# Kernel optimization log

Hardware: AMD Instinct MI355X
Metric: run time of the kernel (lower is better)

Reference implementation:

```python
import jax, jax.numpy as jnp
import numpy as np

E, K, D = 50000, 8, 256
NH = 4
HD = D // NH
SCALE = HD ** -0.5
EPS = 1e-8


def setup_inputs() -> dict:
    key = jax.random.key(0)
    ks = jax.random.split(key, 16)
    p = lambda k, shp: (jax.random.normal(k, shp, dtype=jnp.float32) * 0.02)
    return {
        "x_i": jax.random.normal(ks[0], (E, D), dtype=jnp.float32),
        "x_j": jax.random.normal(ks[1], (E, D), dtype=jnp.float32),
        "h_seq_i": jax.random.normal(ks[2], (E, K, D), dtype=jnp.float32),
        "h_seq_j": jax.random.normal(ks[3], (E, K, D), dtype=jnp.float32),
        "edge_emb": jax.random.normal(ks[4], (E, D), dtype=jnp.float32),
        "Wq": p(ks[5], (D, D)), "bq": jnp.zeros((D,), jnp.float32),
        "Wk": p(ks[6], (D, D)), "bk": jnp.zeros((D,), jnp.float32),
        "We1": p(ks[7], (D, D // 2)), "be1": jnp.zeros((D // 2,), jnp.float32),
        "We2": p(ks[8], (D // 2, 1)), "be2": jnp.zeros((1,), jnp.float32),
        "Wo1": p(ks[9], (3, 16)), "bo1": jnp.zeros((16,), jnp.float32),
        "Wo2": p(ks[10], (16, 1)), "bo2": jnp.zeros((1,), jnp.float32),
    }


def reference(x_i, x_j, h_seq_i, h_seq_j, edge_emb,
              Wq, bq, Wk, bk, We1, be1, We2, be2, Wo1, bo1, Wo2, bo2):
    # (A) attribute alignment: cosine similarity mapped to (0,1)
    num = jnp.sum(x_i * x_j, axis=-1)
    den = jnp.maximum(jnp.linalg.norm(x_i, axis=-1), EPS) * \
          jnp.maximum(jnp.linalg.norm(x_j, axis=-1), EPS)
    attr_score = (num / den + 1.0) / 2.0  # [E]

    # (B) activity alignment: tiny cross-attention, mean of softmax diagonal
    Q = (jnp.einsum('ekd,df->ekf', h_seq_i, Wq) + bq).reshape(E, K, NH, HD)
    Kv = (jnp.einsum('ekd,df->ekf', h_seq_j, Wk) + bk).reshape(E, K, NH, HD)
    scores = jnp.einsum('eqhd,ekhd->ehqk', Q, Kv) * SCALE  # [E,NH,K,K]
    attn = jax.nn.softmax(scores, axis=-1)
    diag = jnp.diagonal(attn, axis1=-2, axis2=-1)  # [E,NH,K]
    activity_score = diag.mean(axis=(-1, -2))  # [E]

    # (C) edge plausibility MLP (exact GELU as in torch default)
    h = jax.nn.gelu(edge_emb @ We1 + be1, approximate=False)
    edge_score = jax.nn.sigmoid((h @ We2 + be2)[..., 0])  # [E]

    signals = jnp.stack([attr_score, activity_score, edge_score], axis=-1)  # [E,3]
    out = jax.nn.gelu(signals @ Wo1 + bo1, approximate=False) @ Wo2 + bo2
    return jax.nn.sigmoid(out[..., 0])  # [E]
```

## Files before the change

### kernel.cpp

```cpp
#include <hip/hip_runtime.h>

#define E_TOT   50000
#define DD      256
#define TE      4
#define NGROUP  (E_TOT / TE)
#define SCALE_V 0.125f

typedef __attribute__((ext_vector_type(4))) float f32x4;
typedef __attribute__((ext_vector_type(8))) short short8;

__device__ __forceinline__ unsigned short f2bf(float f) {
    unsigned u = __float_as_uint(f);
    u += 0x7fffu + ((u >> 16) & 1u);
    return (unsigned short)(u >> 16);
}
__device__ __forceinline__ float gelu_exact(float x) {
    return 0.5f * x * (1.0f + erff(x * 0.70710678118654752440f));
}
__device__ __forceinline__ float sigmoidf(float x) {
    return 1.0f / (1.0f + __expf(-x));
}

__device__ __forceinline__ f32x4 aload(const float* p) {
    f32x4 r;
    asm volatile("global_load_dwordx4 %0, %1, off" : "=v"(r) : "v"(p));
    return r;
}
#define WAITV(N) do { asm volatile("s_waitcnt vmcnt(" #N ")" ::: "memory"); \
                      __builtin_amdgcn_sched_barrier(0); } while (0)

__global__ void prep_weights(const float* __restrict__ Wq,
                             const float* __restrict__ Wk,
                             const float* __restrict__ We1,
                             unsigned short* __restrict__ wqT,
                             unsigned short* __restrict__ wkT,
                             unsigned short* __restrict__ w1T) {
    int i = blockIdx.x * 256 + threadIdx.x;
    if (i < 65536) {
        int k = i >> 8, n = i & 255;
        wqT[n * 256 + k] = f2bf(Wq[i]);
    } else if (i < 131072) {
        int j = i - 65536;
        int k = j >> 8, n = j & 255;
        wkT[n * 256 + k] = f2bf(Wk[j]);
    } else {
        int j = i - 131072;
        int k = j >> 7, n = j & 127;
        w1T[n * 256 + k] = f2bf(We1[j]);
    }
}

__device__ __forceinline__ void proj_gemm(const unsigned short (*A)[260],
                                          const unsigned short* __restrict__ Wt,
                                          f32x4 acc[2][4], int lr, int lq, int w) {
    #pragma unroll
    for (int ks = 0; ks < 8; ++ks) {
        short8 a0 = *(const short8*)&A[lr][ks * 32 + lq * 8];
        short8 a1 = *(const short8*)&A[16 + lr][ks * 32 + lq * 8];
        #pragma unroll
        for (int n = 0; n < 4; ++n) {
            const int col = (w * 4 + n) * 16 + lr;
            short8 bv = *(const short8*)(Wt + col * 256 + ks * 32 + lq * 8);
            acc[0][n] = __builtin_amdgcn_mfma_f32_16x16x32_bf16(a0, bv, acc[0][n], 0, 0, 0);
            acc[1][n] = __builtin_amdgcn_mfma_f32_16x16x32_bf16(a1, bv, acc[1][n], 0, 0, 0);
        }
    }
}

__device__ __forceinline__ void writeback(unsigned short (*T)[260],
                                          const f32x4 acc[2][4],
                                          const float* __restrict__ bias,
                                          int lr, int lq, int w) {
    #pragma unroll
    for (int n = 0; n < 4; ++n) {
        const int col = (w * 4 + n) * 16 + lr;
        const float bs = bias[col];
        #pragma unroll
        for (int m = 0; m < 2; ++m) {
            #pragma unroll
            for (int v = 0; v < 4; ++v) {
                const int row = m * 16 + lq * 4 + v;
                T[row][col] = f2bf(acc[m][n][v] + bs);
            }
        }
    }
}

__global__ __launch_bounds__(256, 3)
void fused_all(const float* __restrict__ x_i,
               const float* __restrict__ x_j,
               const float* __restrict__ h_i,
               const float* __restrict__ h_j,
               const float* __restrict__ emb,
               const unsigned short* __restrict__ wqT,
               const unsigned short* __restrict__ wkT,
               const unsigned short* __restrict__ w1T,
               const float* __restrict__ bq,
               const float* __restrict__ bk,
               const float* __restrict__ be1,
               const float* __restrict__ We2,
               const float* __restrict__ be2,
               const float* __restrict__ Wo1,
               const float* __restrict__ bo1,
               const float* __restrict__ Wo2,
               const float* __restrict__ bo2,
               float* __restrict__ out) {
    __shared__ unsigned short tI[32][260];
    __shared__ unsigned short tJ[32][260];
    __shared__ float sEmb[TE][DD];
    __shared__ float sEdgeP[4][4];

    const int t  = threadIdx.x;
    const int w  = t >> 6;
    const int l  = t & 63;
    const int lr = l & 15, lq = l >> 4;
    const int g  = blockIdx.x;
    const int e  = g * TE + w;
    const size_t hbase = (size_t)g * (TE * 8 * DD);

    f32x4 si[8], sj[8];
    #pragma unroll
    for (int i = 0; i < 8; ++i)
        si[i] = aload(h_i + hbase + (size_t)(i * 256 + t) * 4);
    #pragma unroll
    for (int i = 0; i < 8; ++i)
        sj[i] = aload(h_j + hbase + (size_t)(i * 256 + t) * 4);
    f32x4 xa = aload(x_i + (size_t)e * DD + l * 4);
    f32x4 xb = aload(x_j + (size_t)e * DD + l * 4);
    f32x4 em = aload(emb + ((size_t)g * TE + (t >> 6)) * DD + (t & 63) * 4);
    __builtin_amdgcn_sched_barrier(0);

    WAITV(11);
    #pragma unroll
    for (int i = 0; i < 8; ++i) {
        const int f = i * 256 + t;
        *(ushort4*)&tI[f >> 6][(f & 63) * 4] =
            make_ushort4(f2bf(si[i][0]), f2bf(si[i][1]), f2bf(si[i][2]), f2bf(si[i][3]));
    }
    WAITV(3);
    #pragma unroll
    for (int i = 0; i < 8; ++i) {
        const int f = i * 256 + t;
        *(ushort4*)&tJ[f >> 6][(f & 63) * 4] =
            make_ushort4(f2bf(sj[i][0]), f2bf(sj[i][1]), f2bf(sj[i][2]), f2bf(sj[i][3]));
    }
    WAITV(0);
    *(f32x4*)&sEmb[t >> 6][(t & 63) * 4] = em;
    float cd = xa[0]*xb[0] + xa[1]*xb[1] + xa[2]*xb[2] + xa[3]*xb[3];
    float ci = xa[0]*xa[0] + xa[1]*xa[1] + xa[2]*xa[2] + xa[3]*xa[3];
    float cj = xb[0]*xb[0] + xb[1]*xb[1] + xb[2]*xb[2] + xb[3]*xb[3];
    __syncthreads();

    f32x4 accE[2] = {};
    {
        #pragma unroll
        for (int ks = 0; ks < 8; ++ks) {
            f32x4 e0 = *(const f32x4*)&sEmb[lr & 3][ks * 32 + lq * 8];
            f32x4 e1 = *(const f32x4*)&sEmb[lr & 3][ks * 32 + lq * 8 + 4];
            short8 ae;
            ae[0] = (short)f2bf(e0[0]); ae[1] = (short)f2bf(e0[1]);
            ae[2] = (short)f2bf(e0[2]); ae[3] = (short)f2bf(e0[3]);
            ae[4] = (short)f2bf(e1[0]); ae[5] = (short)f2bf(e1[1]);
            ae[6] = (short)f2bf(e1[2]); ae[7] = (short)f2bf(e1[3]);
            #pragma unroll
            for (int n = 0; n < 2; ++n) {
                const int col = w * 32 + n * 16 + lr;
                short8 bv = *(const short8*)(w1T + col * 256 + ks * 32 + lq * 8);
                accE[n] = __builtin_amdgcn_mfma_f32_16x16x32_bf16(ae, bv, accE[n], 0, 0, 0);
            }
        }
    }
    {
        f32x4 accQ[2][4] = {};
        proj_gemm(tI, wqT, accQ, lr, lq, w);
        __syncthreads();
        writeback(tI, accQ, bq, lr, lq, w);
    }
    {
        f32x4 accK[2][4] = {};
        proj_gemm(tJ, wkT, accK, lr, lq, w);
        __syncthreads();
        writeback(tJ, accK, bk, lr, lq, w);
    }
    {
        float p[4] = {0.f, 0.f, 0.f, 0.f};
        #pragma unroll
        for (int n = 0; n < 2; ++n) {
            const int col = w * 32 + n * 16 + lr;
            const float b1 = be1[col], w2 = We2[col];
            #pragma unroll
            for (int v = 0; v < 4; ++v)
                p[v] += gelu_exact(accE[n][v] + b1) * w2;
        }
        #pragma unroll
        for (int off = 1; off < 16; off <<= 1) {
            #pragma unroll
            for (int v = 0; v < 4; ++v) p[v] += __shfl_xor(p[v], off);
        }
        if (l == 0) {
            sEdgeP[w][0] = p[0]; sEdgeP[w][1] = p[1];
            sEdgeP[w][2] = p[2]; sEdgeP[w][3] = p[3];
        }
    }
    __syncthreads();

    float contrib = 0.f;
    #pragma unroll
    for (int h = 0; h < 4; ++h) {
        f32x4 s = {};
        #pragma unroll
        for (int ks = 0; ks < 2; ++ks) {
            short8 a = *(const short8*)&tJ[w * 8 + (lr & 7)][h * 64 + ks * 32 + lq * 8];
            short8 b = *(const short8*)&tI[w * 8 + (lr & 7)][h * 64 + ks * 32 + lq * 8];
            s = __builtin_amdgcn_mfma_f32_16x16x32_bf16(a, b, s, 0, 0, 0);
        }
        float sc[4];
        #pragma unroll
        for (int v = 0; v < 4; ++v) sc[v] = s[v] * SCALE_V;
        float m4 = fmaxf(fmaxf(sc[0], sc[1]), fmaxf(sc[2], sc[3]));
        float mx = fmaxf(m4, __shfl_xor(m4, 16));
        float pe[4], ps = 0.f;
        #pragma unroll
        for (int v = 0; v < 4; ++v) { pe[v] = __expf(sc[v] - mx); ps += pe[v]; }
        float tot = ps + __shfl_xor(ps, 16);
        float pd = 0.f;
        #pragma unroll
        for (int v = 0; v < 4; ++v)
            pd = (((lq * 4 + v) & 7) == (lr & 7)) ? pe[v] : pd;
        if (lr < 8 && lq < 2) contrib += pd / tot;
    }

    #pragma unroll
    for (int off = 1; off < 64; off <<= 1) {
        contrib += __shfl_xor(contrib, off);
        cd += __shfl_xor(cd, off);
        ci += __shfl_xor(ci, off);
        cj += __shfl_xor(cj, off);
    }
    const float act  = contrib * (1.0f / 32.0f);
    const float attr = (cd / (fmaxf(sqrtf(ci), 1e-8f) * fmaxf(sqrtf(cj), 1e-8f))
                        + 1.0f) * 0.5f;
    const float es = sigmoidf(sEdgeP[0][w] + sEdgeP[1][w] + sEdgeP[2][w] +
                              sEdgeP[3][w] + be2[0]);

    float r = 0.f;
    if (l < 16) {
        float z = attr * Wo1[l] + act * Wo1[16 + l] + es * Wo1[32 + l] + bo1[l];
        r = gelu_exact(z) * Wo2[l];
    }
    r += __shfl_xor(r, 1);
    r += __shfl_xor(r, 2);
    r += __shfl_xor(r, 4);
    r += __shfl_xor(r, 8);
    if (l == 0) out[e] = sigmoidf(r + bo2[0]);
}

extern "C" void kernel_launch(void* const* d_in, const int* in_sizes, int n_in,
                              void* d_out, int out_size, void* d_ws, size_t ws_size,
                              hipStream_t stream) {
    const float* x_i  = (const float*)d_in[0];
    const float* x_j  = (const float*)d_in[1];
    const float* h_i  = (const float*)d_in[2];
    const float* h_j  = (const float*)d_in[3];
    const float* emb  = (const float*)d_in[4];
    const float* Wq   = (const float*)d_in[5];
    const float* bq   = (const float*)d_in[6];
    const float* Wk   = (const float*)d_in[7];
    const float* bk   = (const float*)d_in[8];
    const float* We1  = (const float*)d_in[9];
    const float* be1  = (const float*)d_in[10];
    const float* We2  = (const float*)d_in[11];
    const float* be2  = (const float*)d_in[12];
    const float* Wo1  = (const float*)d_in[13];
    const float* bo1  = (const float*)d_in[14];
    const float* Wo2  = (const float*)d_in[15];
    const float* bo2  = (const float*)d_in[16];
    float* out = (float*)d_out;

    unsigned short* wqT = (unsigned short*)d_ws;
    unsigned short* wkT = wqT + 65536;
    unsigned short* w1T = wkT + 65536;

    prep_weights<<<640, 256, 0, stream>>>(Wq, Wk, We1, wqT, wkT, w1T);
    fused_all<<<NGROUP, 256, 0, stream>>>(x_i, x_j, h_i, h_j, emb,
                                          wqT, wkT, w1T,
                                          bq, bk, be1, We2, be2,
                                          Wo1, bo1, Wo2, bo2, out);
}
```

Measured before the change: 607.5 us.

## Pre-convert activations to bf16 MFMA fragment layout in a separate pass

Adds a conversion kernel that rewrites h_seq_i, h_seq_j and edge_emb into bf16 arrays laid out as MFMA A-fragments in workspace. A new fused kernel then loads these fragments directly from global memory, skipping the LDS staging and conversion, and raises occupancy to 4. The old kernel stays as a fallback when the workspace is too small, with padded sEmb rows. The extra pass adds a full read of the fp32 inputs plus a write and re-read of the bf16 copies.

```diff
diff --git a/kernel.cpp b/kernel.cpp
--- a/kernel.cpp
+++ b/kernel.cpp
@@ -6,6 +6,9 @@
 #define NGROUP  (E_TOT / TE)
 #define SCALE_V 0.125f
 
+#define NHCHUNK 12800000
+#define NECHUNK 1600000
+
 typedef __attribute__((ext_vector_type(4))) float f32x4;
 typedef __attribute__((ext_vector_type(8))) short short8;
 
@@ -20,14 +23,6 @@
 __device__ __forceinline__ float sigmoidf(float x) {
     return 1.0f / (1.0f + __expf(-x));
 }
-
-__device__ __forceinline__ f32x4 aload(const float* p) {
-    f32x4 r;
-    asm volatile("global_load_dwordx4 %0, %1, off" : "=v"(r) : "v"(p));
-    return r;
-}
-#define WAITV(N) do { asm volatile("s_waitcnt vmcnt(" #N ")" ::: "memory"); \
-                      __builtin_amdgcn_sched_barrier(0); } while (0)
 
 __global__ void prep_weights(const float* __restrict__ Wq,
                              const float* __restrict__ Wk,
@@ -50,6 +45,229 @@
     }
 }
 
+__global__ void conv_frag(const float* __restrict__ hi,
+                          const float* __restrict__ hj,
+                          const float* __restrict__ emb,
+                          unsigned short* __restrict__ fi,
+                          unsigned short* __restrict__ fj,
+                          unsigned short* __restrict__ ebf) {
+    const int nthr = gridDim.x * blockDim.x;
+    const int tid  = blockIdx.x * blockDim.x + threadIdx.x;
+
+    for (int c = tid; c < NHCHUNK; c += nthr) {
+        const int g  = c >> 10;
+        const int r  = c & 1023;
+        const int ks = r >> 7, m = (r >> 6) & 1, l = r & 63;
+        const size_t row = (size_t)g * 32 + m * 16 + (l & 15);
+        const int    col = ks * 32 + (l >> 4) * 8;
+        const float* pi = hi + row * DD + col;
+        const float* pj = hj + row * DD + col;
+        f32x4 a0 = *(const f32x4*)pi;
+        f32x4 a1 = *(const f32x4*)(pi + 4);
+        f32x4 b0 = *(const f32x4*)pj;
+        f32x4 b1 = *(const f32x4*)(pj + 4);
+        ushort4 ua0 = make_ushort4(f2bf(a0[0]), f2bf(a0[1]), f2bf(a0[2]), f2bf(a0[3]));
+        ushort4 ua1 = make_ushort4(f2bf(a1[0]), f2bf(a1[1]), f2bf(a1[2]), f2bf(a1[3]));
+        ushort4 ub0 = make_ushort4(f2bf(b0[0]), f2bf(b0[1]), f2bf(b0[2]), f2bf(b0[3]));
+        ushort4 ub1 = make_ushort4(f2bf(b1[0]), f2bf(b1[1]), f2bf(b1[2]), f2bf(b1[3]));
+        *(ushort4*)(fi + (size_t)c * 8)     = ua0;
+        *(ushort4*)(fi + (size_t)c * 8 + 4) = ua1;
+        *(ushort4*)(fj + (size_t)c * 8)     = ub0;
+        *(ushort4*)(fj + (size_t)c * 8 + 4) = ub1;
+    }
+    for (int c = tid; c < NECHUNK; c += nthr) {
+        const float* p = emb + (size_t)c * 8;
+        f32x4 a0 = *(const f32x4*)p;
+        f32x4 a1 = *(const f32x4*)(p + 4);
+        *(ushort4*)(ebf + (size_t)c * 8)     =
+            make_ushort4(f2bf(a0[0]), f2bf(a0[1]), f2bf(a0[2]), f2bf(a0[3]));
+        *(ushort4*)(ebf + (size_t)c * 8 + 4) =
+            make_ushort4(f2bf(a1[0]), f2bf(a1[1]), f2bf(a1[2]), f2bf(a1[3]));
+    }
+}
+
+__device__ __forceinline__ void writeback(unsigned short (*T)[260],
+                                          const f32x4 acc[2][4],
+                                          const float* __restrict__ bias,
+                                          int lr, int lq, int w) {
+    #pragma unroll
+    for (int n = 0; n < 4; ++n) {
+        const int col = (w * 4 + n) * 16 + lr;
+        const float bs = bias[col];
+        #pragma unroll
+        for (int m = 0; m < 2; ++m) {
+            #pragma unroll
+            for (int v = 0; v < 4; ++v) {
+                const int row = m * 16 + lq * 4 + v;
+                T[row][col] = f2bf(acc[m][n][v] + bs);
+            }
+        }
+    }
+}
+
+__global__ __launch_bounds__(256, 4)
+void fused_direct(const float* __restrict__ x_i,
+                  const float* __restrict__ x_j,
+                  const unsigned short* __restrict__ fi,
+                  const unsigned short* __restrict__ fj,
+                  const unsigned short* __restrict__ ebf,
+                  const unsigned short* __restrict__ wqT,
+                  const unsigned short* __restrict__ wkT,
+                  const unsigned short* __restrict__ w1T,
+                  const float* __restrict__ bq,
+                  const float* __restrict__ bk,
+                  const float* __restrict__ be1,
+                  const float* __restrict__ We2,
+                  const float* __restrict__ be2,
+                  const float* __restrict__ Wo1,
+                  const float* __restrict__ bo1,
+                  const float* __restrict__ Wo2,
+                  const float* __restrict__ bo2,
+                  float* __restrict__ out) {
+    __shared__ unsigned short tI[32][260];
+    __shared__ unsigned short tJ[32][260];
+    __shared__ float sEdgeP[4][4];
+
+    const int t  = threadIdx.x;
+    const int w  = t >> 6;
+    const int l  = t & 63;
+    const int lr = l & 15, lq = l >> 4;
+    const int g  = blockIdx.x;
+    const int e  = g * TE + w;
+
+    f32x4 xa = *(const f32x4*)(x_i + (size_t)e * DD + l * 4);
+    f32x4 xb = *(const f32x4*)(x_j + (size_t)e * DD + l * 4);
+    float cd = xa[0]*xb[0] + xa[1]*xb[1] + xa[2]*xb[2] + xa[3]*xb[3];
+    float ci = xa[0]*xa[0] + xa[1]*xa[1] + xa[2]*xa[2] + xa[3]*xa[3];
+    float cj = xb[0]*xb[0] + xb[1]*xb[1] + xb[2]*xb[2] + xb[3]*xb[3];
+
+    {
+        const unsigned short* fb = fi + (size_t)g * 8192;
+        f32x4 acc[2][4] = {};
+        #pragma unroll
+        for (int ks = 0; ks < 8; ++ks) {
+            short8 a0 = *(const short8*)(fb + ks * 1024 + l * 8);
+            short8 a1 = *(const short8*)(fb + ks * 1024 + 512 + l * 8);
+            #pragma unroll
+            for (int n = 0; n < 4; ++n) {
+                const int col = (w * 4 + n) * 16 + lr;
+                short8 bv = *(const short8*)(wqT + col * 256 + ks * 32 + lq * 8);
+                acc[0][n] = __builtin_amdgcn_mfma_f32_16x16x32_bf16(a0, bv, acc[0][n], 0, 0, 0);
+                acc[1][n] = __builtin_amdgcn_mfma_f32_16x16x32_bf16(a1, bv, acc[1][n], 0, 0, 0);
+            }
+        }
+        writeback(tI, acc, bq, lr, lq, w);
+    }
+    {
+        const unsigned short* fb = fj + (size_t)g * 8192;
+        f32x4 acc[2][4] = {};
+        #pragma unroll
+        for (int ks = 0; ks < 8; ++ks) {
+            short8 a0 = *(const short8*)(fb + ks * 1024 + l * 8);
+            short8 a1 = *(const short8*)(fb + ks * 1024 + 512 + l * 8);
+            #pragma unroll
+            for (int n = 0; n < 4; ++n) {
+                const int col = (w * 4 + n) * 16 + lr;
+                short8 bv = *(const short8*)(wkT + col * 256 + ks * 32 + lq * 8);
+                acc[0][n] = __builtin_amdgcn_mfma_f32_16x16x32_bf16(a0, bv, acc[0][n], 0, 0, 0);
+                acc[1][n] = __builtin_amdgcn_mfma_f32_16x16x32_bf16(a1, bv, acc[1][n], 0, 0, 0);
+            }
+        }
+        writeback(tJ, acc, bk, lr, lq, w);
+    }
+    {
+        f32x4 accE[2] = {};
+        const unsigned short* er = ebf + (size_t)g * 1024 + (lr & 3) * 256;
+        #pragma unroll
+        for (int ks = 0; ks < 8; ++ks) {
+            short8 ae = *(const short8*)(er + ks * 32 + lq * 8);
+            #pragma unroll
+            for (int n = 0; n < 2; ++n) {
+                const int col = w * 32 + n * 16 + lr;
+                short8 bv = *(const short8*)(w1T + col * 256 + ks * 32 + lq * 8);
+                accE[n] = __builtin_amdgcn_mfma_f32_16x16x32_bf16(ae, bv, accE[n], 0, 0, 0);
+            }
+        }
+        float p[4] = {0.f, 0.f, 0.f, 0.f};
+        #pragma unroll
+        for (int n = 0; n < 2; ++n) {
+            const int col = w * 32 + n * 16 + lr;
+            const float b1 = be1[col], w2 = We2[col];
+            #pragma unroll
+            for (int v = 0; v < 4; ++v)
+                p[v] += gelu_exact(accE[n][v] + b1) * w2;
+        }
+        #pragma unroll
+        for (int off = 1; off < 16; off <<= 1) {
+            #pragma unroll
+            for (int v = 0; v < 4; ++v) p[v] += __shfl_xor(p[v], off);
+        }
+        if (l == 0) {
+            sEdgeP[w][0] = p[0]; sEdgeP[w][1] = p[1];
+            sEdgeP[w][2] = p[2]; sEdgeP[w][3] = p[3];
+        }
+    }
+    __syncthreads();
+
+    float contrib = 0.f;
+    #pragma unroll
+    for (int h = 0; h < 4; ++h) {
+        f32x4 s = {};
+        #pragma unroll
+        for (int ks = 0; ks < 2; ++ks) {
+            short8 a = *(const short8*)&tJ[w * 8 + (lr & 7)][h * 64 + ks * 32 + lq * 8];
+            short8 b = *(const short8*)&tI[w * 8 + (lr & 7)][h * 64 + ks * 32 + lq * 8];
+            s = __builtin_amdgcn_mfma_f32_16x16x32_bf16(a, b, s, 0, 0, 0);
+        }
+        float sc[4];
+        #pragma unroll
+        for (int v = 0; v < 4; ++v) sc[v] = s[v] * SCALE_V;
+        float m4 = fmaxf(fmaxf(sc[0], sc[1]), fmaxf(sc[2], sc[3]));
+        float mx = fmaxf(m4, __shfl_xor(m4, 16));
+        float pe[4], ps = 0.f;
+        #pragma unroll
+        for (int v = 0; v < 4; ++v) { pe[v] = __expf(sc[v] - mx); ps += pe[v]; }
+        float tot = ps + __shfl_xor(ps, 16);
+        float pd = 0.f;
+        #pragma unroll
+        for (int v = 0; v < 4; ++v)
+            pd = (((lq * 4 + v) & 7) == (lr & 7)) ? pe[v] : pd;
+        if (lr < 8 && lq < 2) contrib += pd / tot;
+    }
+
+    #pragma unroll
+    for (int off = 1; off < 64; off <<= 1) {
+        contrib += __shfl_xor(contrib, off);
+        cd += __shfl_xor(cd, off);
+        ci += __shfl_xor(ci, off);
+        cj += __shfl_xor(cj, off);
+    }
+    const float act  = contrib * (1.0f / 32.0f);
+    const float attr = (cd / (fmaxf(sqrtf(ci), 1e-8f) * fmaxf(sqrtf(cj), 1e-8f))
+                        + 1.0f) * 0.5f;
+    const float es = sigmoidf(sEdgeP[0][w] + sEdgeP[1][w] + sEdgeP[2][w] +
+                              sEdgeP[3][w] + be2[0]);
+
+    float r = 0.f;
+    if (l < 16) {
+        float z = attr * Wo1[l] + act * Wo1[16 + l] + es * Wo1[32 + l] + bo1[l];
+        r = gelu_exact(z) * Wo2[l];
+    }
+    r += __shfl_xor(r, 1);
+    r += __shfl_xor(r, 2);
+    r += __shfl_xor(r, 4);
+    r += __shfl_xor(r, 8);
+    if (l == 0) out[e] = sigmoidf(r + bo2[0]);
+}
+
+__device__ __forceinline__ f32x4 aload(const float* p) {
+    f32x4 r;
+    asm volatile("global_load_dwordx4 %0, %1, off" : "=v"(r) : "v"(p));
+    return r;
+}
+#define WAITV(N) do { asm volatile("s_waitcnt vmcnt(" #N ")" ::: "memory"); \
+                      __builtin_amdgcn_sched_barrier(0); } while (0)
+
 __device__ __forceinline__ void proj_gemm(const unsigned short (*A)[260],
                                           const unsigned short* __restrict__ Wt,
                                           f32x4 acc[2][4], int lr, int lq, int w) {
@@ -67,47 +285,28 @@
     }
 }
 
-__device__ __forceinline__ void writeback(unsigned short (*T)[260],
-                                          const f32x4 acc[2][4],
-                                          const float* __restrict__ bias,
-                                          int lr, int lq, int w) {
-    #pragma unroll
-    for (int n = 0; n < 4; ++n) {
-        const int col = (w * 4 + n) * 16 + lr;
-        const float bs = bias[col];
-        #pragma unroll
-        for (int m = 0; m < 2; ++m) {
-            #pragma unroll
-            for (int v = 0; v < 4; ++v) {
-                const int row = m * 16 + lq * 4 + v;
-                T[row][col] = f2bf(acc[m][n][v] + bs);
-            }
-        }
-    }
-}
-
 __global__ __launch_bounds__(256, 3)
-void fused_all(const float* __restrict__ x_i,
-               const float* __restrict__ x_j,
-               const float* __restrict__ h_i,
-               const float* __restrict__ h_j,
-               const float* __restrict__ emb,
-               const unsigned short* __restrict__ wqT,
-               const unsigned short* __restrict__ wkT,
-               const unsigned short* __restrict__ w1T,
-               const float* __restrict__ bq,
-               const float* __restrict__ bk,
-               const float* __restrict__ be1,
-               const float* __restrict__ We2,
-               const float* __restrict__ be2,
-               const float* __restrict__ Wo1,
-               const float* __restrict__ bo1,
-               const float* __restrict__ Wo2,
-               const float* __restrict__ bo2,
-               float* __restrict__ out) {
+void fused_legacy(const float* __restrict__ x_i,
+                  const float* __restrict__ x_j,
+                  const float* __restrict__ h_i,
+                  const float* __restrict__ h_j,
+                  const float* __restrict__ emb,
+                  const unsigned short* __restrict__ wqT,
+                  const unsigned short* __restrict__ wkT,
+                  const unsigned short* __restrict__ w1T,
+                  const float* __restrict__ bq,
+                  const float* __restrict__ bk,
+                  const float* __restrict__ be1,
+                  const float* __restrict__ We2,
+                  const float* __restrict__ be2,
+                  const float* __restrict__ Wo1,
+                  const float* __restrict__ bo1,
+                  const float* __restrict__ Wo2,
+                  const float* __restrict__ bo2,
+                  float* __restrict__ out) {
     __shared__ unsigned short tI[32][260];
     __shared__ unsigned short tJ[32][260];
-    __shared__ float sEmb[TE][DD];
+    __shared__ float sEmb[TE][DD + 4];
     __shared__ float sEdgeP[4][4];
 
     const int t  = threadIdx.x;
@@ -152,22 +351,20 @@
     __syncthreads();
 
     f32x4 accE[2] = {};
-    {
-        #pragma unroll
-        for (int ks = 0; ks < 8; ++ks) {
-            f32x4 e0 = *(const f32x4*)&sEmb[lr & 3][ks * 32 + lq * 8];
-            f32x4 e1 = *(const f32x4*)&sEmb[lr & 3][ks * 32 + lq * 8 + 4];
-            short8 ae;
-            ae[0] = (short)f2bf(e0[0]); ae[1] = (short)f2bf(e0[1]);
-            ae[2] = (short)f2bf(e0[2]); ae[3] = (short)f2bf(e0[3]);
-            ae[4] = (short)f2bf(e1[0]); ae[5] = (short)f2bf(e1[1]);
-            ae[6] = (short)f2bf(e1[2]); ae[7] = (short)f2bf(e1[3]);
-            #pragma unroll
-            for (int n = 0; n < 2; ++n) {
-                const int col = w * 32 + n * 16 + lr;
-                short8 bv = *(const short8*)(w1T + col * 256 + ks * 32 + lq * 8);
-                accE[n] = __builtin_amdgcn_mfma_f32_16x16x32_bf16(ae, bv, accE[n], 0, 0, 0);
-            }
+    #pragma unroll
+    for (int ks = 0; ks < 8; ++ks) {
+        f32x4 e0 = *(const f32x4*)&sEmb[lr & 3][ks * 32 + lq * 8];
+        f32x4 e1 = *(const f32x4*)&sEmb[lr & 3][ks * 32 + lq * 8 + 4];
+        short8 ae;
+        ae[0] = (short)f2bf(e0[0]); ae[1] = (short)f2bf(e0[1]);
+        ae[2] = (short)f2bf(e0[2]); ae[3] = (short)f2bf(e0[3]);
+        ae[4] = (short)f2bf(e1[0]); ae[5] = (short)f2bf(e1[1]);
+        ae[6] = (short)f2bf(e1[2]); ae[7] = (short)f2bf(e1[3]);
+        #pragma unroll
+        for (int n = 0; n < 2; ++n) {
+            const int col = w * 32 + n * 16 + lr;
+            short8 bv = *(const short8*)(w1T + col * 256 + ks * 32 + lq * 8);
+            accE[n] = __builtin_amdgcn_mfma_f32_16x16x32_bf16(ae, bv, accE[n], 0, 0, 0);
         }
     }
     {
@@ -229,7 +426,6 @@
             pd = (((lq * 4 + v) & 7) == (lr & 7)) ? pe[v] : pd;
         if (lr < 8 && lq < 2) contrib += pd / tot;
     }
-
     #pragma unroll
     for (int off = 1; off < 64; off <<= 1) {
         contrib += __shfl_xor(contrib, off);
@@ -242,7 +438,6 @@
                         + 1.0f) * 0.5f;
     const float es = sigmoidf(sEdgeP[0][w] + sEdgeP[1][w] + sEdgeP[2][w] +
                               sEdgeP[3][w] + be2[0]);
-
     float r = 0.f;
     if (l < 16) {
         float z = attr * Wo1[l] + act * Wo1[16 + l] + es * Wo1[32 + l] + bo1[l];
@@ -280,10 +475,23 @@
     unsigned short* wqT = (unsigned short*)d_ws;
     unsigned short* wkT = wqT + 65536;
     unsigned short* w1T = wkT + 65536;
+    unsigned short* ebf = w1T + 32768;
+    unsigned short* fi  = ebf + 12800000;
+    unsigned short* fj  = fi + 102400000;
+    const size_t need = 131072ull + 131072 + 65536 +
+                        25600000ull + 204800000ull * 2;
 
     prep_weights<<<640, 256, 0, stream>>>(Wq, Wk, We1, wqT, wkT, w1T);
-    fused_all<<<NGROUP, 256, 0, stream>>>(x_i, x_j, h_i, h_j, emb,
-                                          wqT, wkT, w1T,
-                                          bq, bk, be1, We2, be2,
-                                          Wo1, bo1, Wo2, bo2, out);
-}
+    if (ws_size >= need) {
+        conv_frag<<<2048, 256, 0, stream>>>(h_i, h_j, emb, fi, fj, ebf);
+        fused_direct<<<NGROUP, 256, 0, stream>>>(x_i, x_j, fi, fj, ebf,
+                                                 wqT, wkT, w1T,
+                                                 bq, bk, be1, We2, be2,
+                                                 Wo1, bo1, Wo2, bo2, out);
+    } else {
+        fused_legacy<<<NGROUP, 256, 0, stream>>>(x_i, x_j, h_i, h_j, emb,
+                                                 wqT, wkT, w1T,
+                                                 bq, bk, be1, We2, be2,
+                                                 Wo1, bo1, Wo2, bo2, out);
+    }
+}
```

Result: slower. 853.6 us (+40.5%).
